# Kernel optimization log

Hardware: AMD Instinct MI355X
Metric: run time of the kernel (lower is better)

## Reference

```python
import jax, jax.numpy as jnp
import numpy as np

D = 1024
H = 4 * D
E = 8
K = 2


def setup_inputs() -> dict:
    key = jax.random.key(0)
    ks = jax.random.split(key, 8)
    s = 1.0 / np.sqrt(D)
    sh = 1.0 / np.sqrt(H)
    return {
        "x": jax.random.normal(ks[0], (4, 2048, D), dtype=jnp.float32),
        "gate_w": jax.random.uniform(ks[1], (D, E), jnp.float32, -s, s),
        "gate_b": jax.random.uniform(ks[2], (E,), jnp.float32, -s, s),
        "w1": jax.random.uniform(ks[3], (E, D, H), jnp.float32, -s, s),
        "b1": jax.random.uniform(ks[4], (E, H), jnp.float32, -s, s),
        "w2": jax.random.uniform(ks[5], (E, H, D), jnp.float32, -sh, sh),
        "b2": jax.random.uniform(ks[6], (E, D), jnp.float32, -sh, sh),
    }


def reference(x, gate_w, gate_b, w1, b1, w2, b2):
    # Gating: softmax over experts, top-k, renormalize.
    gate_logits = jnp.einsum("bsd,de->bse", x, gate_w) + gate_b
    weights = jax.nn.softmax(gate_logits, axis=-1)
    top_w, top_idx = jax.lax.top_k(weights, K)  # [B,S,K]
    top_w = top_w / jnp.sum(top_w, axis=-1, keepdims=True)

    out = jnp.zeros_like(x)
    # Loop over the fixed, small set of experts; dense FFN per expert,
    # masked-weighted combine (same math as the per-token torch loop).
    for e in range(E):
        # combine weight for expert e per token: sum of top_w where selected
        w_e = jnp.sum(jnp.where(top_idx == e, top_w, 0.0), axis=-1)  # [B,S]
        h = jax.nn.gelu(jnp.einsum("bsd,dh->bsh", x, w1[e]) + b1[e], approximate=False)
        y = jnp.einsum("bsh,hd->bsd", h, w2[e]) + b2[e]
        out = out + w_e[..., None] * y
    return out
```

## Files before the change

kernel.cpp:

```cpp
#include <hip/hip_runtime.h>
#include <math.h>

#define T_TOK 8192
#define DDIM  1024
#define HDIM  4096
#define NEXP  8
#define BM    128
#define BN    128
#define BK    64
#define MAXROWS (T_TOK*2 + NEXP*BM)
#define MAXTILES (MAXROWS/BM)
#define KS2   2
#define NGATE (T_TOK/8)
#define NTR1  ((HDIM/64)*(DDIM/64)*NEXP)
#define NTR2  ((DDIM/64)*(HDIM/64)*NEXP)

typedef __attribute__((ext_vector_type(8))) short short8;
typedef __attribute__((ext_vector_type(4))) short short4v;
typedef __attribute__((ext_vector_type(4))) float f32x4;

typedef const __attribute__((address_space(1))) unsigned int* gp1_t;
typedef __attribute__((address_space(3))) unsigned int* lp3_t;

__device__ __forceinline__ void gld16(const void* g, void* l) {
  __builtin_amdgcn_global_load_lds((gp1_t)g, (lp3_t)l, 16, 0, 0);
}

__device__ __forceinline__ short f2bf(float f) {
  unsigned u = __float_as_uint(f);
  u += 0x7fffu + ((u >> 16) & 1u);
  return (short)(u >> 16);
}

__device__ __forceinline__ void tr_body(float* sl ,
    const float* __restrict__ w, short* __restrict__ wt, int R, int C, int lb) {
  int ctiles = C / 64, rtiles = R / 64;
  int e  = lb / (ctiles * rtiles);
  int rm = lb % (ctiles * rtiles);
  int r0 = (rm / ctiles) * 64;
  int c0 = (rm % ctiles) * 64;
  const float* W = w + (size_t)e * R * C;
  short* O = wt + (size_t)e * R * C;
  int t = threadIdx.x;
  int lr = t >> 4, lc4 = (t & 15) * 4;
#pragma unroll
  for (int i = 0; i < 4; i++) {
    float4 v = *(const float4*)&W[(size_t)(r0 + lr + i * 16) * C + c0 + lc4];
    sl[(lr + i * 16) * 65 + lc4 + 0] = v.x;
    sl[(lr + i * 16) * 65 + lc4 + 1] = v.y;
    sl[(lr + i * 16) * 65 + lc4 + 2] = v.z;
    sl[(lr + i * 16) * 65 + lc4 + 3] = v.w;
  }
  __syncthreads();
#pragma unroll
  for (int i = 0; i < 4; i++) {
    int oc = lr + i * 16;
    short4v s;
#pragma unroll
    for (int j = 0; j < 4; j++) s[j] = f2bf(sl[(lc4 + j) * 65 + oc]);
    *(short4v*)&O[(size_t)(c0 + oc) * R + r0 + lc4] = s;
  }
}

__device__ __forceinline__ void gate_body(char* smem, int bid,
    const float* __restrict__ x, const float* __restrict__ gw,
    const float* __restrict__ gb, int2* __restrict__ toke,
    float2* __restrict__ tokw, int* __restrict__ bcnt, short* __restrict__ xb) {
  float* sg = (float*)smem;
  int* lcnt = (int*)(smem + NEXP * DDIM * 4);
  int t = threadIdx.x;
#pragma unroll
  for (int it = 0; it < 8; ++it) {
    int l0 = (it * 256 + t) * 4;
    float4 v = *(const float4*)&gw[l0];
    int d = l0 >> 3, e0 = l0 & 7;
    sg[(e0 + 0) * DDIM + d] = v.x;
    sg[(e0 + 1) * DDIM + d] = v.y;
    sg[(e0 + 2) * DDIM + d] = v.z;
    sg[(e0 + 3) * DDIM + d] = v.w;
  }
  if (t < NEXP) lcnt[t] = 0;
  __syncthreads();
  int wave = t >> 6, lane = t & 63;
  int tok0 = bid * 8 + wave * 2;
#pragma unroll
  for (int tk = 0; tk < 2; ++tk) {
    int tok = tok0 + tk;
    float p[NEXP];
#pragma unroll
    for (int e = 0; e < NEXP; e++) p[e] = 0.f;
#pragma unroll
    for (int c = 0; c < 4; c++) {
      int d = c * 256 + lane * 4;
      float4 xv = *(const float4*)&x[(size_t)tok * DDIM + d];
      short4v sv;
      sv[0] = f2bf(xv.x); sv[1] = f2bf(xv.y); sv[2] = f2bf(xv.z); sv[3] = f2bf(xv.w);
      *(short4v*)&xb[(size_t)tok * DDIM + d] = sv;
#pragma unroll
      for (int e = 0; e < NEXP; e++) {
        float4 g = *(const float4*)&sg[e * DDIM + d];
        p[e] += xv.x * g.x + xv.y * g.y + xv.z * g.z + xv.w * g.w;
      }
    }
#pragma unroll
    for (int off = 32; off; off >>= 1)
#pragma unroll
      for (int e = 0; e < NEXP; e++) p[e] += __shfl_xor(p[e], off);
    if (lane == 0) {
      float l[NEXP];
#pragma unroll
      for (int e = 0; e < NEXP; e++) l[e] = p[e] + gb[e];
      int i0 = 0;
#pragma unroll
      for (int e = 1; e < NEXP; e++) if (l[e] > l[i0]) i0 = e;
      int i1 = (i0 == 0) ? 1 : 0;
#pragma unroll
      for (int e = 0; e < NEXP; e++) if (e != i0 && l[e] > l[i1]) i1 = e;
      float ex = expf(l[i1] - l[i0]);
      float w0 = 1.f / (1.f + ex);
      toke[tok] = make_int2(i0, i1);
      tokw[tok] = make_float2(w0, 1.f - w0);
      atomicAdd(&lcnt[i0], 1);
      atomicAdd(&lcnt[i1], 1);
    }
  }
  __syncthreads();
  if (t < NEXP) bcnt[bid * NEXP + t] = lcnt[t];
}

__global__ __launch_bounds__(256) void k_front(const float* __restrict__ x,
    const float* __restrict__ gw, const float* __restrict__ gb,
    const float* __restrict__ w1, const float* __restrict__ w2,
    int2* __restrict__ toke, float2* __restrict__ tokw, int* __restrict__ bcnt,
    short* __restrict__ xb, short* __restrict__ w1t, short* __restrict__ w2t) {
  __shared__ char smem[NEXP * DDIM * 4 + 64];
  int bid = blockIdx.x;
  if (bid < NGATE) {
    gate_body(smem, bid, x, gw, gb, toke, tokw, bcnt, xb);
  } else if (bid < NGATE + NTR1) {
    tr_body((float*)smem, w1, w1t, DDIM, HDIM, bid - NGATE);
  } else {
    tr_body((float*)smem, w2, w2t, HDIM, DDIM, bid - NGATE - NTR1);
  }
}

__global__ __launch_bounds__(256) void k_plan(const int* __restrict__ bcnt,
    int* __restrict__ pbase, int* __restrict__ texp) {
  __shared__ int tot[NEXP];
  __shared__ int b[NEXP + 1];
  int t = threadIdx.x;
  if (t < NEXP) tot[t] = 0;
  __syncthreads();
  int e = t & 7, sum = 0;
  for (int i = t >> 3; i < NGATE; i += 32) sum += bcnt[i * NEXP + e];
  atomicAdd(&tot[e], sum);
  __syncthreads();
  if (t == 0) {
    b[0] = 0;
#pragma unroll
    for (int ee = 0; ee < NEXP; ee++)
      b[ee + 1] = b[ee] + ((tot[ee] + BM - 1) & ~(BM - 1));
#pragma unroll
    for (int ee = 0; ee < NEXP; ee++) pbase[ee] = b[ee];
  }
  __syncthreads();
  for (int i = t; i < MAXTILES; i += 256) {
    int r0 = i * BM, ee = -1;
#pragma unroll
    for (int k = 0; k < NEXP; k++) if (r0 >= b[k] && r0 < b[k + 1]) ee = k;
    texp[i] = ee;
  }
}

__global__ __launch_bounds__(256) void k_scatter(const int2* __restrict__ toke,
    const float2* __restrict__ tokw, const int* __restrict__ pbase,
    int* __restrict__ fill, int* __restrict__ rtok, float* __restrict__ rwgt) {
  int tok = blockIdx.x * 256 + threadIdx.x;
  if (tok >= T_TOK) return;
  int2 te = toke[tok];
  float2 tw = tokw[tok];
  int s0 = atomicAdd(&fill[te.x], 1);
  rtok[pbase[te.x] + s0] = tok; rwgt[pbase[te.x] + s0] = tw.x;
  int s1 = atomicAdd(&fill[te.y], 1);
  rtok[pbase[te.y] + s1] = tok; rwgt[pbase[te.y] + s1] = tw.y;
}


#define STG(ko) { \
  gld16(sA[0] + (ko), &AL[(0 * 32 + wid * 8) * BK]); \
  gld16(sA[1] + (ko), &AL[(1 * 32 + wid * 8) * BK]); \
  gld16(sA[2] + (ko), &AL[(2 * 32 + wid * 8) * BK]); \
  gld16(sA[3] + (ko), &AL[(3 * 32 + wid * 8) * BK]); \
  gld16(sB[0] + (ko), &BL[(0 * 32 + wid * 8) * BK]); \
  gld16(sB[1] + (ko), &BL[(1 * 32 + wid * 8) * BK]); \
  gld16(sB[2] + (ko), &BL[(2 * 32 + wid * 8) * BK]); \
  gld16(sB[3] + (ko), &BL[(3 * 32 + wid * 8) * BK]); }

#define MFMA_TILE { \
  __builtin_amdgcn_s_setprio(1); \
  _Pragma("unroll") \
  for (int s = 0; s < 2; ++s) { \
    int xo = ((s * 4 + kg) ^ x7) << 3; \
    short8 af[4], bg[4]; \
    _Pragma("unroll") \
    for (int i = 0; i < 4; i++) af[i] = *(short8*)&AL[(wm + i * 16 + lr) * BK + xo]; \
    _Pragma("unroll") \
    for (int j = 0; j < 4; j++) bg[j] = *(short8*)&BL[(wn + j * 16 + lr) * BK + xo]; \
    _Pragma("unroll") \
    for (int i = 0; i < 4; i++) \
    _Pragma("unroll") \
    for (int j = 0; j < 4; j++) \
      acc[i][j] = __builtin_amdgcn_mfma_f32_16x16x32_bf16(af[i], bg[j], acc[i][j], 0, 0, 0); \
  } \
  __builtin_amdgcn_s_setprio(0); }

#define GEMM_LOOP(NKv) \
  for (int kt = 0; kt < (NKv); ++kt) { \
    STG(kt * BK); \
    asm volatile("s_waitcnt vmcnt(0)" ::: "memory"); \
    __syncthreads(); \
    MFMA_TILE; \
    __syncthreads(); \
  }

__global__ __launch_bounds__(256, 4) void k_ffn1(const short* __restrict__ xb,
    const short* __restrict__ w1t, const float* __restrict__ b1,
    const int* __restrict__ rtok, const int* __restrict__ texp,
    int tile_base, short* __restrict__ hbuf) {
  int tl = blockIdx.y;
  int tm = tile_base + tl;
  int e = texp[tm];
  if (e < 0) return;
  int n0 = blockIdx.x * BN;
  const short* W = w1t + (size_t)e * HDIM * DDIM;
  __shared__ short LDSBUF[2 * BM * BK];
  short* AL = LDSBUF;
  short* BL = LDSBUF + BM * BK;
  int t = threadIdx.x, wid = t >> 6, lane = t & 63;
  int sr8 = lane >> 3, slot = lane & 7;
  int swz = (slot ^ sr8) * 8;
  const short* sA[4]; const short* sB[4];
#pragma unroll
  for (int i = 0; i < 4; i++) {
    int r = i * 32 + wid * 8 + sr8;
    int tok = rtok[tm * BM + r]; if (tok < 0) tok = 0;
    sA[i] = xb + (size_t)tok * DDIM + swz;
    sB[i] = W + (size_t)(n0 + r) * DDIM + swz;
  }

  f32x4 acc[4][4];
#pragma unroll
  for (int i = 0; i < 4; i++)
#pragma unroll
    for (int j = 0; j < 4; j++) acc[i][j] = (f32x4){0.f, 0.f, 0.f, 0.f};

  int wm = (wid >> 1) * 64, wn = (wid & 1) * 64;
  int lr = lane & 15, kg = lane >> 4, x7 = lr & 7;

  GEMM_LOOP(DDIM / BK)

  short* SB = LDSBUF + wid * (32 * 68);
#pragma unroll
  for (int p = 0; p < 2; ++p) {
#pragma unroll
    for (int i2 = 0; i2 < 2; ++i2) {
      int i = p * 2 + i2;
#pragma unroll
      for (int j = 0; j < 4; ++j) {
        int col = j * 16 + lr;
        float bias = b1[e * HDIM + n0 + wn + col];
#pragma unroll
        for (int r = 0; r < 4; ++r) {
          float v = acc[i][j][r] + bias;
          v = 0.5f * v * (1.f + erff(v * 0.70710678118f));
          SB[(i2 * 16 + kg * 4 + r) * 68 + col] = f2bf(v);
        }
      }
    }
    int lrow = lane >> 1, c0 = (lane & 1) * 32;
    size_t grow = (size_t)(tl * BM + wm + p * 32 + lrow);
#pragma unroll
    for (int s = 0; s < 4; ++s) {
      short8 v = *(short8*)&SB[lrow * 68 + c0 + s * 8];
      *(short8*)&hbuf[grow * HDIM + n0 + wn + c0 + s * 8] = v;
    }
  }
}

__global__ __launch_bounds__(256, 4) void k_ffn2(const short* __restrict__ hbuf,
    const short* __restrict__ w2t, const float* __restrict__ b2,
    const int* __restrict__ rtok, const float* __restrict__ rwgt,
    const int* __restrict__ texp, int tile_base, float* __restrict__ out) {
  int tl = blockIdx.z;
  int tm = tile_base + tl;
  int e = texp[tm];
  if (e < 0) return;
  int kc = blockIdx.y;
  int n0 = blockIdx.x * BN;
  const short* W = w2t + (size_t)e * DDIM * HDIM;
  __shared__ short LDSBUF[2 * BM * BK];
  short* AL = LDSBUF;
  short* BL = LDSBUF + BM * BK;
  int t = threadIdx.x, wid = t >> 6, lane = t & 63;
  int sr8 = lane >> 3, slot = lane & 7;
  int swz = (slot ^ sr8) * 8;
  const int NK = HDIM / BK / KS2;
  int kbase = kc * NK * BK;
  const short* sA[4]; const short* sB[4];
#pragma unroll
  for (int i = 0; i < 4; i++) {
    int r = i * 32 + wid * 8 + sr8;
    sA[i] = hbuf + (size_t)(tl * BM + r) * HDIM + kbase + swz;
    sB[i] = W + (size_t)(n0 + r) * HDIM + kbase + swz;
  }

  f32x4 acc[4][4];
#pragma unroll
  for (int i = 0; i < 4; i++)
#pragma unroll
    for (int j = 0; j < 4; j++) acc[i][j] = (f32x4){0.f, 0.f, 0.f, 0.f};

  int wm = (wid >> 1) * 64, wn = (wid & 1) * 64;
  int lr = lane & 15, kg = lane >> 4, x7 = lr & 7;

  GEMM_LOOP(NK)

#pragma unroll
  for (int j = 0; j < 4; j++) {
    int gcol = n0 + wn + j * 16 + lr;
    float bias = (kc == 0) ? b2[e * DDIM + gcol] : 0.f;
#pragma unroll
    for (int i = 0; i < 4; i++) {
      int rl = wm + i * 16 + kg * 4;
#pragma unroll
      for (int r = 0; r < 4; r++) {
        int grow = tm * BM + rl + r;
        int tok = rtok[grow];
        if (tok >= 0) {
          float v = (acc[i][j][r] + bias) * rwgt[grow];
          atomicAdd(&out[(size_t)tok * DDIM + gcol], v);
        }
      }
    }
  }
}

extern "C" void kernel_launch(void* const* d_in, const int* in_sizes, int n_in,
                              void* d_out, int out_size, void* d_ws, size_t ws_size,
                              hipStream_t stream) {
  const float* x  = (const float*)d_in[0];
  const float* gw = (const float*)d_in[1];
  const float* gb = (const float*)d_in[2];
  const float* w1 = (const float*)d_in[3];
  const float* b1 = (const float*)d_in[4];
  const float* w2 = (const float*)d_in[5];
  const float* b2 = (const float*)d_in[6];
  float* out = (float*)d_out;
  char* ws = (char*)d_ws;

  int*    fill  = (int*)(ws + 32);
  int*    pbase = (int*)(ws + 64);
  int*    texp  = (int*)(ws + 128);
  int*    rtok  = (int*)(ws + 1024);
  float*  rwgt  = (float*)(ws + 1024 + (size_t)MAXROWS * 4);
  int2*   toke  = (int2*)(ws + 1024 + (size_t)MAXROWS * 8);
  float2* tokw  = (float2*)(ws + 1024 + (size_t)MAXROWS * 8 + (size_t)T_TOK * 8);
  int*    bcnt  = (int*)(ws + 640 * 1024);
  size_t wbytes = (size_t)NEXP * DDIM * HDIM * 2;
  short*  w1t   = (short*)(ws + (1 << 20));
  short*  w2t   = (short*)(ws + (1 << 20) + wbytes);
  short*  xb    = (short*)(ws + (1 << 20) + 2 * wbytes);
  size_t hoff   = (1 << 20) + 2 * wbytes + (size_t)T_TOK * DDIM * 2;
  short*  hbuf  = (short*)(ws + hoff);

  size_t hcap = ws_size > hoff ? ws_size - hoff : 0;
  int tpc = (int)(hcap / ((size_t)BM * HDIM * 2));
  if (tpc < 1) return;
  if (tpc > MAXTILES) tpc = MAXTILES;

  hipMemsetAsync(d_out, 0, (size_t)T_TOK * DDIM * 4, stream);
  hipMemsetAsync(ws, 0, 128, stream);
  hipMemsetAsync(rtok, 0xFF, (size_t)MAXROWS * 4, stream);

  k_front<<<NGATE + NTR1 + NTR2, 256, 0, stream>>>(x, gw, gb, w1, w2,
                                                   toke, tokw, bcnt, xb, w1t, w2t);
  k_plan<<<1, 256, 0, stream>>>(bcnt, pbase, texp);
  k_scatter<<<T_TOK / 256, 256, 0, stream>>>(toke, tokw, pbase, fill, rtok, rwgt);

  for (int base = 0; base < MAXTILES; base += tpc) {
    int nt = MAXTILES - base;
    if (nt > tpc) nt = tpc;
    k_ffn1<<<dim3(HDIM / BN, nt), 256, 0, stream>>>(xb, w1t, b1, rtok, texp, base, hbuf);
    k_ffn2<<<dim3(DDIM / BN, KS2, nt), 256, 0, stream>>>(hbuf, w2t, b2, rtok, rwgt,
                                                         texp, base, out);
  }
}
```

Baseline: 645.7 us.

## Replace atomic scatter in FFN2 with dense per-row output and gather combine

When the workspace is large enough, the second GEMM runs with no K-split and writes each routed row's FP32 result to a dense buffer, staged through LDS for coalesced stores. A new combine kernel then gathers each token's two expert rows, adds bias and applies the gate weights, which removes the output memset and the atomic accumulation into the output. It also swaps erff in GELU for a polynomial erf approximation (Abramowitz-Stegun, max error about 1.5e-7) to cut epilogue math. The cost is an extra round trip through a large intermediate buffer, fewer blocks in FFN2 without the K-split, and a small accuracy change in GELU.

```diff
diff --git a/kernel.cpp b/kernel.cpp
--- a/kernel.cpp
+++ b/kernel.cpp
@@ -32,6 +32,15 @@
   return (short)(u >> 16);
 }
 
+__device__ __forceinline__ float erf_fast(float x) {
+  float ax = fabsf(x);
+  float t = 1.f / (1.f + 0.3275911f * ax);
+  float poly = t * (0.254829592f + t * (-0.284496736f + t * (1.421413741f +
+               t * (-1.453152027f + t * 1.061405429f))));
+  float r = 1.f - poly * __expf(-ax * ax);
+  return copysignf(r, x);
+}
+
 __device__ __forceinline__ void tr_body(float* sl ,
     const float* __restrict__ w, short* __restrict__ wt, int R, int C, int lb) {
   int ctiles = C / 64, rtiles = R / 64;
@@ -174,15 +183,40 @@
 
 __global__ __launch_bounds__(256) void k_scatter(const int2* __restrict__ toke,
     const float2* __restrict__ tokw, const int* __restrict__ pbase,
-    int* __restrict__ fill, int* __restrict__ rtok, float* __restrict__ rwgt) {
+    int* __restrict__ fill, int* __restrict__ rtok, float* __restrict__ rwgt,
+    int* __restrict__ trow) {
   int tok = blockIdx.x * 256 + threadIdx.x;
   if (tok >= T_TOK) return;
   int2 te = toke[tok];
   float2 tw = tokw[tok];
   int s0 = atomicAdd(&fill[te.x], 1);
-  rtok[pbase[te.x] + s0] = tok; rwgt[pbase[te.x] + s0] = tw.x;
+  int r0 = pbase[te.x] + s0;
+  rtok[r0] = tok; rwgt[r0] = tw.x; trow[tok * 2] = r0;
   int s1 = atomicAdd(&fill[te.y], 1);
-  rtok[pbase[te.y] + s1] = tok; rwgt[pbase[te.y] + s1] = tw.y;
+  int r1 = pbase[te.y] + s1;
+  rtok[r1] = tok; rwgt[r1] = tw.y; trow[tok * 2 + 1] = r1;
+}
+
+__global__ __launch_bounds__(256) void k_out(const float* __restrict__ out2,
+    const float* __restrict__ b2, const int2* __restrict__ toke,
+    const float2* __restrict__ tokw, const int* __restrict__ trow,
+    float* __restrict__ out) {
+  int idx = blockIdx.x * 256 + threadIdx.x;
+  int tok = idx >> 8;
+  int seg = (idx & 255) * 4;
+  int2 te = toke[tok];
+  float2 tw = tokw[tok];
+  int r0 = trow[tok * 2], r1 = trow[tok * 2 + 1];
+  float4 a  = *(const float4*)&out2[(size_t)r0 * DDIM + seg];
+  float4 c  = *(const float4*)&out2[(size_t)r1 * DDIM + seg];
+  float4 p0 = *(const float4*)&b2[te.x * DDIM + seg];
+  float4 p1 = *(const float4*)&b2[te.y * DDIM + seg];
+  float4 o;
+  o.x = tw.x * (a.x + p0.x) + tw.y * (c.x + p1.x);
+  o.y = tw.x * (a.y + p0.y) + tw.y * (c.y + p1.y);
+  o.z = tw.x * (a.z + p0.z) + tw.y * (c.z + p1.z);
+  o.w = tw.x * (a.w + p0.w) + tw.y * (c.w + p1.w);
+  *(float4*)&out[(size_t)tok * DDIM + seg] = o;
 }
 
 
@@ -272,7 +306,7 @@
 #pragma unroll
         for (int r = 0; r < 4; ++r) {
           float v = acc[i][j][r] + bias;
-          v = 0.5f * v * (1.f + erff(v * 0.70710678118f));
+          v = 0.5f * v * (1.f + erf_fast(v * 0.70710678118f));
           SB[(i2 * 16 + kg * 4 + r) * 68 + col] = f2bf(v);
         }
       }
@@ -287,7 +321,59 @@
   }
 }
 
-__global__ __launch_bounds__(256, 4) void k_ffn2(const short* __restrict__ hbuf,
+__global__ __launch_bounds__(256, 4) void k_ffn2d(const short* __restrict__ hbuf,
+    const short* __restrict__ w2t, const int* __restrict__ texp,
+    int tile_base, float* __restrict__ out2) {
+  int tl = blockIdx.y;
+  int tm = tile_base + tl;
+  int e = texp[tm];
+  if (e < 0) return;
+  int n0 = blockIdx.x * BN;
+  const short* W = w2t + (size_t)e * DDIM * HDIM;
+  __shared__ short LDSBUF[2 * BM * BK];
+  short* AL = LDSBUF;
+  short* BL = LDSBUF + BM * BK;
+  int t = threadIdx.x, wid = t >> 6, lane = t & 63;
+  int sr8 = lane >> 3, slot = lane & 7;
+  int swz = (slot ^ sr8) * 8;
+  const short* sA[4]; const short* sB[4];
+#pragma unroll
+  for (int i = 0; i < 4; i++) {
+    int r = i * 32 + wid * 8 + sr8;
+    sA[i] = hbuf + (size_t)(tl * BM + r) * HDIM + swz;
+    sB[i] = W + (size_t)(n0 + r) * HDIM + swz;
+  }
+
+  f32x4 acc[4][4];
+#pragma unroll
+  for (int i = 0; i < 4; i++)
+#pragma unroll
+    for (int j = 0; j < 4; j++) acc[i][j] = (f32x4){0.f, 0.f, 0.f, 0.f};
+
+  int wm = (wid >> 1) * 64, wn = (wid & 1) * 64;
+  int lr = lane & 15, kg = lane >> 4, x7 = lr & 7;
+
+  GEMM_LOOP(HDIM / BK)
+
+  float* SBf = (float*)LDSBUF + wid * (16 * 68);
+#pragma unroll
+  for (int i = 0; i < 4; ++i) {
+#pragma unroll
+    for (int j = 0; j < 4; ++j)
+#pragma unroll
+      for (int r = 0; r < 4; ++r)
+        SBf[(kg * 4 + r) * 68 + j * 16 + lr] = acc[i][j][r];
+    int lrow = lane >> 2, c0 = (lane & 3) * 16;
+    size_t grow = (size_t)(tm * BM + wm + i * 16 + lrow);
+#pragma unroll
+    for (int s = 0; s < 4; ++s) {
+      float4 v = *(float4*)&SBf[lrow * 68 + c0 + s * 4];
+      *(float4*)&out2[grow * DDIM + n0 + wn + c0 + s * 4] = v;
+    }
+  }
+}
+
+__global__ __launch_bounds__(256, 4) void k_ffn2a(const short* __restrict__ hbuf,
     const short* __restrict__ w2t, const float* __restrict__ b2,
     const int* __restrict__ rtok, const float* __restrict__ rwgt,
     const int* __restrict__ texp, int tile_base, float* __restrict__ out) {
@@ -313,13 +399,11 @@
     sA[i] = hbuf + (size_t)(tl * BM + r) * HDIM + kbase + swz;
     sB[i] = W + (size_t)(n0 + r) * HDIM + kbase + swz;
   }
-
   f32x4 acc[4][4];
 #pragma unroll
   for (int i = 0; i < 4; i++)
 #pragma unroll
     for (int j = 0; j < 4; j++) acc[i][j] = (f32x4){0.f, 0.f, 0.f, 0.f};
-
   int wm = (wid >> 1) * 64, wn = (wid & 1) * 64;
   int lr = lane & 15, kg = lane >> 4, x7 = lr & 7;
 
@@ -366,32 +450,45 @@
   int2*   toke  = (int2*)(ws + 1024 + (size_t)MAXROWS * 8);
   float2* tokw  = (float2*)(ws + 1024 + (size_t)MAXROWS * 8 + (size_t)T_TOK * 8);
   int*    bcnt  = (int*)(ws + 640 * 1024);
+  int*    trow  = (int*)(ws + 768 * 1024);
   size_t wbytes = (size_t)NEXP * DDIM * HDIM * 2;
   short*  w1t   = (short*)(ws + (1 << 20));
   short*  w2t   = (short*)(ws + (1 << 20) + wbytes);
   short*  xb    = (short*)(ws + (1 << 20) + 2 * wbytes);
-  size_t hoff   = (1 << 20) + 2 * wbytes + (size_t)T_TOK * DDIM * 2;
-  short*  hbuf  = (short*)(ws + hoff);
-
-  size_t hcap = ws_size > hoff ? ws_size - hoff : 0;
-  int tpc = (int)(hcap / ((size_t)BM * HDIM * 2));
-  if (tpc < 1) return;
-  if (tpc > MAXTILES) tpc = MAXTILES;
-
-  hipMemsetAsync(d_out, 0, (size_t)T_TOK * DDIM * 4, stream);
+  size_t xend   = (1 << 20) + 2 * wbytes + (size_t)T_TOK * DDIM * 2;
+  size_t o2b    = (size_t)MAXROWS * DDIM * 4;
+  size_t hbytes = (size_t)MAXTILES * BM * HDIM * 2;
+
+  bool dense = ws_size >= xend + o2b + hbytes;
+
   hipMemsetAsync(ws, 0, 128, stream);
   hipMemsetAsync(rtok, 0xFF, (size_t)MAXROWS * 4, stream);
 
   k_front<<<NGATE + NTR1 + NTR2, 256, 0, stream>>>(x, gw, gb, w1, w2,
                                                    toke, tokw, bcnt, xb, w1t, w2t);
   k_plan<<<1, 256, 0, stream>>>(bcnt, pbase, texp);
-  k_scatter<<<T_TOK / 256, 256, 0, stream>>>(toke, tokw, pbase, fill, rtok, rwgt);
-
-  for (int base = 0; base < MAXTILES; base += tpc) {
-    int nt = MAXTILES - base;
-    if (nt > tpc) nt = tpc;
-    k_ffn1<<<dim3(HDIM / BN, nt), 256, 0, stream>>>(xb, w1t, b1, rtok, texp, base, hbuf);
-    k_ffn2<<<dim3(DDIM / BN, KS2, nt), 256, 0, stream>>>(hbuf, w2t, b2, rtok, rwgt,
-                                                         texp, base, out);
-  }
-}
+  k_scatter<<<T_TOK / 256, 256, 0, stream>>>(toke, tokw, pbase, fill, rtok, rwgt, trow);
+
+  if (dense) {
+    float* out2 = (float*)(ws + xend);
+    short* hbuf = (short*)(ws + xend + o2b);
+    k_ffn1<<<dim3(HDIM / BN, MAXTILES), 256, 0, stream>>>(xb, w1t, b1, rtok, texp,
+                                                          0, hbuf);
+    k_ffn2d<<<dim3(DDIM / BN, MAXTILES), 256, 0, stream>>>(hbuf, w2t, texp, 0, out2);
+    k_out<<<(T_TOK * DDIM / 4) / 256, 256, 0, stream>>>(out2, b2, toke, tokw, trow, out);
+  } else {
+    short* hbuf = (short*)(ws + xend);
+    size_t hcap = ws_size > xend ? ws_size - xend : 0;
+    int tpc = (int)(hcap / ((size_t)BM * HDIM * 2));
+    if (tpc < 1) return;
+    if (tpc > MAXTILES) tpc = MAXTILES;
+    hipMemsetAsync(d_out, 0, (size_t)T_TOK * DDIM * 4, stream);
+    for (int base = 0; base < MAXTILES; base += tpc) {
+      int nt = MAXTILES - base;
+      if (nt > tpc) nt = tpc;
+      k_ffn1<<<dim3(HDIM / BN, nt), 256, 0, stream>>>(xb, w1t, b1, rtok, texp, base, hbuf);
+      k_ffn2a<<<dim3(DDIM / BN, KS2, nt), 256, 0, stream>>>(hbuf, w2t, b2, rtok, rwgt,
+                                                            texp, base, out);
+    }
+  }
+}
```

New measurement: 588.8 us. -8.8%, faster.
